# Optimization experiments

Hardware: AMD Instinct MI355X
Metric: run time of the kernel (lower is better)

The kernel has to match this reference:

```python
import jax, jax.numpy as jnp
import numpy as np

D = 768      # hidden_size
H = 12       # num_head
HD = D // H  # head_dim
LN_EPS = 1e-5


def setup_inputs() -> dict:
    key = jax.random.key(0)
    ks = jax.random.split(key, 9)
    N, S = 4, 2048
    s = 0.02
    return {
        "hidden_state": jax.random.normal(ks[0], (N, S, D), dtype=jnp.float32),
        "key_padding_mask": jax.random.randint(ks[1], (N, S), 0, 2, dtype=jnp.int64),
        "Wq": jax.random.normal(ks[2], (D, D), dtype=jnp.float32) * s,
        "Wk": jax.random.normal(ks[3], (D, D), dtype=jnp.float32) * s,
        "Wv": jax.random.normal(ks[4], (D, D), dtype=jnp.float32) * s,
        "Wo": jax.random.normal(ks[5], (D, D), dtype=jnp.float32) * s,
        "W1": jax.random.normal(ks[6], (4 * D, D), dtype=jnp.float32) * s,
        "W2": jax.random.normal(ks[7], (D, 4 * D), dtype=jnp.float32) * s,
        "ln_g": jnp.ones((D,), dtype=jnp.float32),
        "ln_b": jnp.zeros((D,), dtype=jnp.float32),
    }


def _layernorm(x, g, b):
    mu = jnp.mean(x, axis=-1, keepdims=True)
    var = jnp.mean(jnp.square(x - mu), axis=-1, keepdims=True)
    return (x - mu) * jax.lax.rsqrt(var + LN_EPS) * g + b


def reference(hidden_state, key_padding_mask, Wq, Wk, Wv, Wo, W1, W2, ln_g, ln_b):
    x = hidden_state
    N, S, _ = x.shape
    # Note: original module projects K and V from `query` (self-attention).
    def proj(W):
        return (x @ W.T).reshape(N, S, H, HD).transpose(0, 2, 1, 3)  # [N,H,S,HD]
    Q, K, V = proj(Wq), proj(Wk), proj(Wv)
    scores = jnp.einsum("bhqd,bhkd->bhqk", Q, K)  # [N,H,S,S]
    # int mask: 0 marks padding positions -> masked with -inf
    pad = (key_padding_mask == 0)[:, None, None, :]  # [N,1,1,S]
    scores = jnp.where(pad, -jnp.inf, scores)
    attn = jax.nn.softmax(scores / np.sqrt(HD), axis=-1)
    ctx = jnp.einsum("bhqk,bhkd->bhqd", attn, V)
    ctx = ctx.transpose(0, 2, 1, 3).reshape(N, S, D)
    mha = ctx @ Wo.T
    # residual + LayerNorm (same LN params used twice, as in the original)
    n1 = _layernorm(x + mha, ln_g, ln_b)
    # FFN with exact GELU (torch nn.GELU default)
    f = jax.nn.gelu(n1 @ W1.T, approximate=False) @ W2.T
    return _layernorm(n1 + f, ln_g, ln_b)
```

## Files before the change

kernel.cpp:

```cpp
#include <hip/hip_runtime.h>
#include <math.h>

typedef unsigned short u16;
typedef unsigned int u32;
typedef __bf16 bf16x8 __attribute__((ext_vector_type(8)));
typedef float f32x4 __attribute__((ext_vector_type(4)));

#define NB 4
#define SS 2048
#define DD 768
#define HH 12
#define HD 64
#define ROWS (NB*SS)

__device__ __forceinline__ u16 f2bf(float f) {
    union { float f; unsigned u; } v; v.f = f;
    unsigned r = v.u + 0x7fffu + ((v.u >> 16) & 1u);
    return (u16)(r >> 16);
}
__device__ __forceinline__ u32 fas(float f) { union { float f; u32 u; } v; v.f = f; return v.u; }

__device__ __forceinline__ void gl_lds16(const void* g, void* l) {
    __builtin_amdgcn_global_load_lds((__attribute__((address_space(1))) void*)(g),
                                     (__attribute__((address_space(3))) void*)(l),
                                     16, 0, 0);
}

__global__ __launch_bounds__(256) void prep_kernel(
        const float* __restrict__ X, const float* __restrict__ Wq,
        const float* __restrict__ Wk, const float* __restrict__ Wv,
        const float* __restrict__ Wo, const float* __restrict__ W1,
        const float* __restrict__ W2, const int* __restrict__ mask,
        u16* __restrict__ Xb, u16* __restrict__ Wqkvb, u16* __restrict__ Wob,
        u16* __restrict__ W1b, u16* __restrict__ W2b, float* __restrict__ mb) {
    const int blk = blockIdx.x, tid = threadIdx.x;
    const float* src; u16* dst; int idx;
    if (blk < 6144)       { src = X;  dst = Xb;               idx = blk * 1024 + tid * 4; }
    else if (blk < 6720)  { src = Wq; dst = Wqkvb;            idx = (blk - 6144) * 1024 + tid * 4; }
    else if (blk < 7296)  { src = Wk; dst = Wqkvb + DD * DD;  idx = (blk - 6720) * 1024 + tid * 4; }
    else if (blk < 7872)  { src = Wv; dst = Wqkvb + 2*DD*DD;  idx = (blk - 7296) * 1024 + tid * 4; }
    else if (blk < 8448)  { src = Wo; dst = Wob;              idx = (blk - 7872) * 1024 + tid * 4; }
    else if (blk < 10752) { src = W1; dst = W1b;              idx = (blk - 8448) * 1024 + tid * 4; }
    else if (blk < 13056) { src = W2; dst = W2b;              idx = (blk - 10752) * 1024 + tid * 4; }
    else {
        int i = (blk - 13056) * 1024 + tid * 4;
        float4 o;
        o.x = mask[i]     == 0 ? -1e30f : 0.0f;
        o.y = mask[i + 1] == 0 ? -1e30f : 0.0f;
        o.z = mask[i + 2] == 0 ? -1e30f : 0.0f;
        o.w = mask[i + 3] == 0 ? -1e30f : 0.0f;
        *(float4*)&mb[i] = o;
        return;
    }
    float4 v = *(const float4*)&src[idx];
    ushort4 o;
    o.x = f2bf(v.x); o.y = f2bf(v.y); o.z = f2bf(v.z); o.w = f2bf(v.w);
    *(ushort4*)&dst[idx] = o;
}

template <int EPI, int BN>
__global__ __launch_bounds__(256) void gemm_bt(const u16* __restrict__ A,
                                               const u16* __restrict__ B,
                                               int M, int N, int K,
                                               void* __restrict__ out,
                                               const void* __restrict__ aux,
                                               u16* __restrict__ Qb,
                                               u16* __restrict__ Kb,
                                               u16* __restrict__ Vb) {
    __shared__ __align__(16) u16 lA[128 * 64];
    __shared__ __align__(16) u16 lB[BN * 64];
    constexpr int MI = (BN == 128) ? 4 : 2;
    const int tid = threadIdx.x;
    const int lane = tid & 63, wave = tid >> 6;
    const int quad = lane >> 4, lc = lane & 15;
    const int xcd = blockIdx.x & 7, loc = blockIdx.x >> 3;
    const int mb = xcd * 8 + (loc & 7), nb = loc >> 3;
    const int m0 = mb * 128, n0 = nb * BN;
    const int wrow = (BN == 128) ? (wave >> 1) * 64 : wave * 32;
    const int wcol = (BN == 128) ? (wave & 1) * 64 : 0;
    const int swz = lc & 7;

    f32x4 acc[MI][4] = {};

    for (int kb = 0; kb < K; kb += 64) {
        __syncthreads();
#pragma unroll
        for (int p0 = 0; p0 < 1024; p0 += 256) {
            int p = p0 + tid, row = p >> 3, cl = (p & 7) ^ (row & 7);
            gl_lds16(A + (size_t)(m0 + row) * K + kb + cl * 8, &lA[(size_t)(p0 + wave * 64) * 8]);
        }
#pragma unroll
        for (int p0 = 0; p0 < BN * 8; p0 += 256) {
            int p = p0 + tid, row = p >> 3, cl = (p & 7) ^ (row & 7);
            gl_lds16(B + (size_t)(n0 + row) * K + kb + cl * 8, &lB[(size_t)(p0 + wave * 64) * 8]);
        }
        __syncthreads();
#pragma unroll
        for (int k2 = 0; k2 < 2; ++k2) {
            bf16x8 af[MI], bfr[4];
#pragma unroll
            for (int t = 0; t < MI; ++t)
                af[t] = *(const bf16x8*)&lA[(wrow + t * 16 + lc) * 64 + ((quad + k2 * 4) ^ swz) * 8];
#pragma unroll
            for (int t = 0; t < 4; ++t)
                bfr[t] = *(const bf16x8*)&lB[(wcol + t * 16 + lc) * 64 + ((quad + k2 * 4) ^ swz) * 8];
#pragma unroll
            for (int mi = 0; mi < MI; ++mi)
#pragma unroll
                for (int ni = 0; ni < 4; ++ni)
                    acc[mi][ni] = __builtin_amdgcn_mfma_f32_16x16x32_bf16(af[mi], bfr[ni],
                                                                         acc[mi][ni], 0, 0, 0);
        }
    }

#pragma unroll
    for (int mi = 0; mi < MI; ++mi) {
#pragma unroll
        for (int r = 0; r < 4; ++r) {
            int m = m0 + wrow + mi * 16 + quad * 4 + r;
#pragma unroll
            for (int ni = 0; ni < 4; ++ni) {
                int n = n0 + wcol + ni * 16 + lc;
                float v = acc[mi][ni][r];
                if constexpr (EPI == 0) {
                    int b = m >> 11, s = m & 2047;
                    int which = n / DD, rem = n - which * DD;
                    int h = rem >> 6, d = rem & 63;
                    u16* dst = which == 0 ? Qb : (which == 1 ? Kb : Vb);
                    dst[((((size_t)b * HH + h) * SS + s) << 6) + d] = f2bf(v);
                } else if constexpr (EPI == 1) {
                    float u = v * fmaf(v * v, 0.035677408f, 0.7978845608f);
                    float e = __builtin_amdgcn_exp2f(u * 2.885390082f);
                    float g = v - v * __builtin_amdgcn_rcpf(e + 1.0f);
                    ((u16*)out)[(size_t)m * N + n] = f2bf(g);
                } else if constexpr (EPI == 2) {
                    ((float*)out)[(size_t)m * N + n] =
                        v + ((const float*)aux)[(size_t)m * N + n];
                } else {
                    ((float*)out)[(size_t)m * N + n] =
                        v + (float)(((const __bf16*)aux)[(size_t)m * N + n]);
                }
            }
        }
    }
}

__global__ __launch_bounds__(256) void transpose_v(const u16* __restrict__ V,
                                                   u16* __restrict__ Vt) {
    __shared__ u16 t[32][33];
    int bh = blockIdx.z;
    int s0 = blockIdx.x * 32, d0 = blockIdx.y * 32;
    const u16* vb = V + (size_t)bh * SS * HD;
    u16* vtb = Vt + (size_t)bh * HD * SS;
    int tx = threadIdx.x & 31, ty = threadIdx.x >> 5;
#pragma unroll
    for (int i = 0; i < 32; i += 8) t[ty + i][tx] = vb[(size_t)(s0 + ty + i) * HD + d0 + tx];
    __syncthreads();
#pragma unroll
    for (int i = 0; i < 32; i += 8) vtb[(size_t)(d0 + ty + i) * SS + s0 + tx] = t[tx][ty + i];
}

__global__ __launch_bounds__(256) void attn_kernel(const u16* __restrict__ Q,
                                                   const u16* __restrict__ K,
                                                   const u16* __restrict__ Vt,
                                                   const float* __restrict__ maskbias,
                                                   u16* __restrict__ Ctx) {
    __shared__ __align__(16) u16 lK[64 * 64];
    __shared__ __align__(16) u16 lV[64 * 64];
    __shared__ __align__(16) u16 lP[4][32 * 72];
    const int tid = threadIdx.x, lane = tid & 63, wave = tid >> 6;
    const int quad = lane >> 4, lc = lane & 15;
    const int bh = blockIdx.x % (NB * HH);
    const int b = bh / HH, h = bh - b * HH;
    const int q0 = (blockIdx.x / (NB * HH)) * 128;
    const u16* Qg = Q + ((size_t)bh * SS + q0 + wave * 32) * HD;
    const u16* Kg = K + (size_t)bh * SS * HD;
    const u16* Vg = Vt + (size_t)bh * HD * SS;
    const float* mbg = maskbias + b * SS;
    const int sw = lc & 7;

    const int srow = tid >> 3, scl = (tid & 7) ^ (srow & 7);
    const int srow2 = (256 + tid) >> 3, scl2 = (tid & 7) ^ (srow2 & 7);

    bf16x8 qf[2][2];
#pragma unroll
    for (int mi = 0; mi < 2; ++mi)
#pragma unroll
        for (int k2 = 0; k2 < 2; ++k2)
            qf[mi][k2] = *(const bf16x8*)(Qg + (size_t)(mi * 16 + lc) * HD + k2 * 32 + quad * 8);

    bf16x8 onesf;
#pragma unroll
    for (int i = 0; i < 8; ++i) onesf[i] = (__bf16)1.0f;

    f32x4 oacc[2][4] = {};
    f32x4 lsum[2] = {};

    for (int j0 = 0; j0 < SS; j0 += 64) {
        __syncthreads();
        gl_lds16(Kg + (size_t)(j0 + srow) * HD + scl * 8,   &lK[(size_t)(wave * 64) * 8]);
        gl_lds16(Vg + (size_t)srow * SS + j0 + scl * 8,     &lV[(size_t)(wave * 64) * 8]);
        gl_lds16(Kg + (size_t)(j0 + srow2) * HD + scl2 * 8, &lK[(size_t)(256 + wave * 64) * 8]);
        gl_lds16(Vg + (size_t)srow2 * SS + j0 + scl2 * 8,   &lV[(size_t)(256 + wave * 64) * 8]);
        __syncthreads();

        f32x4 sacc[4][2] = {};
#pragma unroll
        for (int k2 = 0; k2 < 2; ++k2)
#pragma unroll
            for (int ni = 0; ni < 4; ++ni) {
                bf16x8 kf = *(const bf16x8*)&lK[(ni * 16 + lc) * 64 + ((quad + k2 * 4) ^ sw) * 8];
                sacc[ni][0] = __builtin_amdgcn_mfma_f32_16x16x32_bf16(kf, qf[0][k2], sacc[ni][0], 0, 0, 0);
                sacc[ni][1] = __builtin_amdgcn_mfma_f32_16x16x32_bf16(kf, qf[1][k2], sacc[ni][1], 0, 0, 0);
            }

#pragma unroll
        for (int ni = 0; ni < 4; ++ni) {
            f32x4 mbv = *(const f32x4*)(mbg + j0 + ni * 16 + quad * 4);
#pragma unroll
            for (int mi = 0; mi < 2; ++mi) {
#pragma unroll
                for (int r = 0; r < 4; ++r)
                    sacc[ni][mi][r] = __builtin_amdgcn_exp2f(fmaf(sacc[ni][mi][r], 0.180336880f, mbv[r]));
                u32 w0 = __builtin_amdgcn_perm(fas(sacc[ni][mi][1]), fas(sacc[ni][mi][0]), 0x07060302);
                u32 w1 = __builtin_amdgcn_perm(fas(sacc[ni][mi][3]), fas(sacc[ni][mi][2]), 0x07060302);
                *(uint2*)&lP[wave][(mi * 16 + lc) * 72 + ni * 16 + quad * 4] = make_uint2(w0, w1);
            }
        }

#pragma unroll
        for (int k2 = 0; k2 < 2; ++k2) {
            bf16x8 pf0 = *(const bf16x8*)&lP[wave][(size_t)lc * 72 + k2 * 32 + quad * 8];
            bf16x8 pf1 = *(const bf16x8*)&lP[wave][(size_t)(16 + lc) * 72 + k2 * 32 + quad * 8];
            lsum[0] = __builtin_amdgcn_mfma_f32_16x16x32_bf16(pf0, onesf, lsum[0], 0, 0, 0);
            lsum[1] = __builtin_amdgcn_mfma_f32_16x16x32_bf16(pf1, onesf, lsum[1], 0, 0, 0);
#pragma unroll
            for (int ni = 0; ni < 4; ++ni) {
                bf16x8 vf = *(const bf16x8*)&lV[(ni * 16 + lc) * 64 + ((quad + k2 * 4) ^ sw) * 8];
                oacc[0][ni] = __builtin_amdgcn_mfma_f32_16x16x32_bf16(pf0, vf, oacc[0][ni], 0, 0, 0);
                oacc[1][ni] = __builtin_amdgcn_mfma_f32_16x16x32_bf16(pf1, vf, oacc[1][ni], 0, 0, 0);
            }
        }
    }

#pragma unroll
    for (int mi = 0; mi < 2; ++mi)
#pragma unroll
        for (int r = 0; r < 4; ++r) {
            float inv = 1.0f / lsum[mi][r];
            int s = q0 + wave * 32 + mi * 16 + quad * 4 + r;
            size_t base = ((size_t)(b * SS + s)) * DD + h * HD;
#pragma unroll
            for (int ni = 0; ni < 4; ++ni)
                Ctx[base + ni * 16 + lc] = f2bf(oacc[mi][ni][r] * inv);
        }
}

__global__ __launch_bounds__(256) void ln_kernel(const float* __restrict__ in,
                                                 const float* __restrict__ g,
                                                 const float* __restrict__ bb,
                                                 u16* __restrict__ out_bf,
                                                 float* __restrict__ out_f) {
    const int row = blockIdx.x, tid = threadIdx.x;
    const float* x = in + (size_t)row * DD;
    float v0 = x[tid], v1 = x[tid + 256], v2 = x[tid + 512];
    float s = v0 + v1 + v2;
    float q = v0 * v0 + v1 * v1 + v2 * v2;
#pragma unroll
    for (int o = 1; o < 64; o <<= 1) {
        s += __shfl_xor(s, o);
        q += __shfl_xor(q, o);
    }
    __shared__ float rs[4], rq[4];
    int wave = tid >> 6;
    if ((tid & 63) == 0) { rs[wave] = s; rq[wave] = q; }
    __syncthreads();
    s = rs[0] + rs[1] + rs[2] + rs[3];
    q = rq[0] + rq[1] + rq[2] + rq[3];
    float mu = s * (1.0f / DD);
    float var = q * (1.0f / DD) - mu * mu;
    float rstd = rsqrtf(var + 1e-5f);
#pragma unroll
    for (int j = 0; j < 3; ++j) {
        int col = tid + j * 256;
        float v = (j == 0 ? v0 : (j == 1 ? v1 : v2));
        float y = (v - mu) * rstd * g[col] + bb[col];
        if (out_bf) out_bf[(size_t)row * DD + col] = f2bf(y);
        if (out_f) out_f[(size_t)row * DD + col] = y;
    }
}

extern "C" void kernel_launch(void* const* d_in, const int* in_sizes, int n_in,
                              void* d_out, int out_size, void* d_ws, size_t ws_size,
                              hipStream_t stream) {
    const float* X    = (const float*)d_in[0];
    const int*   mask = (const int*)d_in[1];
    const float* Wq   = (const float*)d_in[2];
    const float* Wk   = (const float*)d_in[3];
    const float* Wv   = (const float*)d_in[4];
    const float* Wo   = (const float*)d_in[5];
    const float* W1   = (const float*)d_in[6];
    const float* W2   = (const float*)d_in[7];
    const float* ln_g = (const float*)d_in[8];
    const float* ln_b = (const float*)d_in[9];
    float* out = (float*)d_out;

    char* ws = (char*)d_ws;
    size_t off = 0;
    auto alloc = [&](size_t bytes) {
        void* p = ws + off;
        off += (bytes + 255) & ~(size_t)255;
        return p;
    };
    u16*   Xbf   = (u16*)alloc((size_t)ROWS * DD * 2);
    u16*   Wqkvb = (u16*)alloc((size_t)3 * DD * DD * 2);
    u16*   Wob   = (u16*)alloc((size_t)DD * DD * 2);
    u16*   W1b   = (u16*)alloc((size_t)4 * DD * DD * 2);
    u16*   W2b   = (u16*)alloc((size_t)4 * DD * DD * 2);
    float* mbias = (float*)alloc((size_t)NB * SS * 4);
    u16*   Qb    = (u16*)alloc((size_t)ROWS * DD * 2);
    u16*   Kb    = (u16*)alloc((size_t)ROWS * DD * 2);
    u16*   Vb    = (u16*)alloc((size_t)ROWS * DD * 2);
    u16*   Vtb   = (u16*)alloc((size_t)ROWS * DD * 2);
    float* resid = (float*)alloc((size_t)ROWS * DD * 4);
    u16*   n1b   = (u16*)alloc((size_t)ROWS * DD * 2);
    u16*   Gb    = Qb;
    u16*   Ctxb  = Xbf;
    float* h2    = resid;

    prep_kernel<<<dim3(13064), dim3(256), 0, stream>>>(
        X, Wq, Wk, Wv, Wo, W1, W2, mask,
        Xbf, Wqkvb, Wob, W1b, W2b, mbias);

    gemm_bt<0, 128><<<dim3((3 * DD / 128) * (ROWS / 128)), dim3(256), 0, stream>>>(
        Xbf, Wqkvb, ROWS, 3 * DD, DD, nullptr, nullptr, Qb, Kb, Vb);

    transpose_v<<<dim3(SS / 32, HD / 32, NB * HH), dim3(256), 0, stream>>>(Vb, Vtb);

    attn_kernel<<<dim3((SS / 128) * (NB * HH)), dim3(256), 0, stream>>>(
        Qb, Kb, Vtb, mbias, Ctxb);

    gemm_bt<2, 64><<<dim3((DD / 64) * (ROWS / 128)), dim3(256), 0, stream>>>(
        Ctxb, Wob, ROWS, DD, DD, resid, X, nullptr, nullptr, nullptr);

    ln_kernel<<<dim3(ROWS), dim3(256), 0, stream>>>(resid, ln_g, ln_b, n1b, nullptr);

    gemm_bt<1, 128><<<dim3((4 * DD / 128) * (ROWS / 128)), dim3(256), 0, stream>>>(
        n1b, W1b, ROWS, 4 * DD, DD, Gb, nullptr, nullptr, nullptr, nullptr);

    gemm_bt<3, 64><<<dim3((DD / 64) * (ROWS / 128)), dim3(256), 0, stream>>>(
        Gb, W2b, ROWS, DD, 4 * DD, h2, n1b, nullptr, nullptr, nullptr);

    ln_kernel<<<dim3(ROWS), dim3(256), 0, stream>>>(h2, ln_g, ln_b, nullptr, out);
}
```

Measured before the change: 364.7 us.

## Use 8 waves per attention block and pass P through permlane swaps instead of LDS

```diff
diff --git a/kernel.cpp b/kernel.cpp
--- a/kernel.cpp
+++ b/kernel.cpp
@@ -5,6 +5,7 @@
 typedef unsigned int u32;
 typedef __bf16 bf16x8 __attribute__((ext_vector_type(8)));
 typedef float f32x4 __attribute__((ext_vector_type(4)));
+typedef u32 u32x4 __attribute__((ext_vector_type(4)));
 
 #define NB 4
 #define SS 2048
@@ -160,100 +161,96 @@
     for (int i = 0; i < 32; i += 8) vtb[(size_t)(d0 + ty + i) * SS + s0 + tx] = t[tx][ty + i];
 }
 
-__global__ __launch_bounds__(256) void attn_kernel(const u16* __restrict__ Q,
-                                                   const u16* __restrict__ K,
-                                                   const u16* __restrict__ Vt,
-                                                   const float* __restrict__ maskbias,
-                                                   u16* __restrict__ Ctx) {
+__global__ __launch_bounds__(512, 6) void attn_kernel(const u16* __restrict__ Q,
+                                                      const u16* __restrict__ K,
+                                                      const u16* __restrict__ Vt,
+                                                      const float* __restrict__ maskbias,
+                                                      u16* __restrict__ Ctx) {
     __shared__ __align__(16) u16 lK[64 * 64];
     __shared__ __align__(16) u16 lV[64 * 64];
-    __shared__ __align__(16) u16 lP[4][32 * 72];
     const int tid = threadIdx.x, lane = tid & 63, wave = tid >> 6;
     const int quad = lane >> 4, lc = lane & 15;
     const int bh = blockIdx.x % (NB * HH);
     const int b = bh / HH, h = bh - b * HH;
     const int q0 = (blockIdx.x / (NB * HH)) * 128;
-    const u16* Qg = Q + ((size_t)bh * SS + q0 + wave * 32) * HD;
+    const u16* Qg = Q + ((size_t)bh * SS + q0 + wave * 16) * HD;
     const u16* Kg = K + (size_t)bh * SS * HD;
     const u16* Vg = Vt + (size_t)bh * HD * SS;
     const float* mbg = maskbias + b * SS;
     const int sw = lc & 7;
 
     const int srow = tid >> 3, scl = (tid & 7) ^ (srow & 7);
-    const int srow2 = (256 + tid) >> 3, scl2 = (tid & 7) ^ (srow2 & 7);
-
-    bf16x8 qf[2][2];
-#pragma unroll
-    for (int mi = 0; mi < 2; ++mi)
-#pragma unroll
-        for (int k2 = 0; k2 < 2; ++k2)
-            qf[mi][k2] = *(const bf16x8*)(Qg + (size_t)(mi * 16 + lc) * HD + k2 * 32 + quad * 8);
+
+    bf16x8 qf[2];
+#pragma unroll
+    for (int k2 = 0; k2 < 2; ++k2)
+        qf[k2] = *(const bf16x8*)(Qg + (size_t)lc * HD + k2 * 32 + quad * 8);
 
     bf16x8 onesf;
 #pragma unroll
     for (int i = 0; i < 8; ++i) onesf[i] = (__bf16)1.0f;
 
-    f32x4 oacc[2][4] = {};
-    f32x4 lsum[2] = {};
+    f32x4 oacc[4] = {};
+    f32x4 lsum = {};
 
     for (int j0 = 0; j0 < SS; j0 += 64) {
         __syncthreads();
-        gl_lds16(Kg + (size_t)(j0 + srow) * HD + scl * 8,   &lK[(size_t)(wave * 64) * 8]);
-        gl_lds16(Vg + (size_t)srow * SS + j0 + scl * 8,     &lV[(size_t)(wave * 64) * 8]);
-        gl_lds16(Kg + (size_t)(j0 + srow2) * HD + scl2 * 8, &lK[(size_t)(256 + wave * 64) * 8]);
-        gl_lds16(Vg + (size_t)srow2 * SS + j0 + scl2 * 8,   &lV[(size_t)(256 + wave * 64) * 8]);
+        gl_lds16(Kg + (size_t)(j0 + srow) * HD + scl * 8, &lK[(size_t)(wave * 64) * 8]);
+        gl_lds16(Vg + (size_t)srow * SS + j0 + scl * 8,   &lV[(size_t)(wave * 64) * 8]);
         __syncthreads();
 
-        f32x4 sacc[4][2] = {};
+        f32x4 sacc[4] = {};
+        __builtin_amdgcn_s_setprio(1);
 #pragma unroll
         for (int k2 = 0; k2 < 2; ++k2)
 #pragma unroll
             for (int ni = 0; ni < 4; ++ni) {
                 bf16x8 kf = *(const bf16x8*)&lK[(ni * 16 + lc) * 64 + ((quad + k2 * 4) ^ sw) * 8];
-                sacc[ni][0] = __builtin_amdgcn_mfma_f32_16x16x32_bf16(kf, qf[0][k2], sacc[ni][0], 0, 0, 0);
-                sacc[ni][1] = __builtin_amdgcn_mfma_f32_16x16x32_bf16(kf, qf[1][k2], sacc[ni][1], 0, 0, 0);
+                sacc[ni] = __builtin_amdgcn_mfma_f32_16x16x32_bf16(kf, qf[k2], sacc[ni], 0, 0, 0);
             }
-
+        __builtin_amdgcn_s_setprio(0);
+
+        u32 pa[4], pb[4];
 #pragma unroll
         for (int ni = 0; ni < 4; ++ni) {
             f32x4 mbv = *(const f32x4*)(mbg + j0 + ni * 16 + quad * 4);
 #pragma unroll
-            for (int mi = 0; mi < 2; ++mi) {
-#pragma unroll
-                for (int r = 0; r < 4; ++r)
-                    sacc[ni][mi][r] = __builtin_amdgcn_exp2f(fmaf(sacc[ni][mi][r], 0.180336880f, mbv[r]));
-                u32 w0 = __builtin_amdgcn_perm(fas(sacc[ni][mi][1]), fas(sacc[ni][mi][0]), 0x07060302);
-                u32 w1 = __builtin_amdgcn_perm(fas(sacc[ni][mi][3]), fas(sacc[ni][mi][2]), 0x07060302);
-                *(uint2*)&lP[wave][(mi * 16 + lc) * 72 + ni * 16 + quad * 4] = make_uint2(w0, w1);
-            }
+            for (int r = 0; r < 4; ++r)
+                sacc[ni][r] = __builtin_amdgcn_exp2f(fmaf(sacc[ni][r], 0.180336880f, mbv[r]));
+            pa[ni] = __builtin_amdgcn_perm(fas(sacc[ni][1]), fas(sacc[ni][0]), 0x07060302);
+            pb[ni] = __builtin_amdgcn_perm(fas(sacc[ni][3]), fas(sacc[ni][2]), 0x07060302);
         }
 
 #pragma unroll
         for (int k2 = 0; k2 < 2; ++k2) {
-            bf16x8 pf0 = *(const bf16x8*)&lP[wave][(size_t)lc * 72 + k2 * 32 + quad * 8];
-            bf16x8 pf1 = *(const bf16x8*)&lP[wave][(size_t)(16 + lc) * 72 + k2 * 32 + quad * 8];
-            lsum[0] = __builtin_amdgcn_mfma_f32_16x16x32_bf16(pf0, onesf, lsum[0], 0, 0, 0);
-            lsum[1] = __builtin_amdgcn_mfma_f32_16x16x32_bf16(pf1, onesf, lsum[1], 0, 0, 0);
+            u32 xa = pa[2 * k2], ya = pa[2 * k2 + 1];
+            u32 xb = pb[2 * k2], yb = pb[2 * k2 + 1];
+            asm("v_permlane32_swap_b32 %0, %1" : "+v"(xa), "+v"(ya));
+            asm("v_permlane16_swap_b32 %0, %1" : "+v"(xa), "+v"(ya));
+            asm("v_permlane32_swap_b32 %0, %1" : "+v"(xb), "+v"(yb));
+            asm("v_permlane16_swap_b32 %0, %1" : "+v"(xb), "+v"(yb));
+            u32x4 pw = { xa, xb, ya, yb };
+            bf16x8 pf = __builtin_bit_cast(bf16x8, pw);
+            __builtin_amdgcn_s_setprio(1);
+            lsum = __builtin_amdgcn_mfma_f32_16x16x32_bf16(pf, onesf, lsum, 0, 0, 0);
 #pragma unroll
             for (int ni = 0; ni < 4; ++ni) {
                 bf16x8 vf = *(const bf16x8*)&lV[(ni * 16 + lc) * 64 + ((quad + k2 * 4) ^ sw) * 8];
-                oacc[0][ni] = __builtin_amdgcn_mfma_f32_16x16x32_bf16(pf0, vf, oacc[0][ni], 0, 0, 0);
-                oacc[1][ni] = __builtin_amdgcn_mfma_f32_16x16x32_bf16(pf1, vf, oacc[1][ni], 0, 0, 0);
+                oacc[ni] = __builtin_amdgcn_mfma_f32_16x16x32_bf16(pf, vf, oacc[ni], 0, 0, 0);
             }
-        }
-    }
-
-#pragma unroll
-    for (int mi = 0; mi < 2; ++mi)
-#pragma unroll
-        for (int r = 0; r < 4; ++r) {
-            float inv = 1.0f / lsum[mi][r];
-            int s = q0 + wave * 32 + mi * 16 + quad * 4 + r;
-            size_t base = ((size_t)(b * SS + s)) * DD + h * HD;
-#pragma unroll
-            for (int ni = 0; ni < 4; ++ni)
-                Ctx[base + ni * 16 + lc] = f2bf(oacc[mi][ni][r] * inv);
-        }
+            __builtin_amdgcn_s_setprio(0);
+        }
+    }
+
+#pragma unroll
+    for (int r = 0; r < 4; ++r) {
+        float inv = 1.0f / lsum[r];
+        int s = q0 + wave * 16 + quad * 4 + r;
+        size_t base = ((size_t)(b * SS + s)) * DD + h * HD;
+#pragma unroll
+        for (int ni = 0; ni < 4; ++ni)
+            Ctx[base + ni * 16 + lc] = f2bf(oacc[ni][r] * inv);
+    }
 }
 
 __global__ __launch_bounds__(256) void ln_kernel(const float* __restrict__ in,
@@ -337,7 +334,7 @@
 
     transpose_v<<<dim3(SS / 32, HD / 32, NB * HH), dim3(256), 0, stream>>>(Vb, Vtb);
 
-    attn_kernel<<<dim3((SS / 128) * (NB * HH)), dim3(256), 0, stream>>>(
+    attn_kernel<<<dim3((SS / 128) * (NB * HH)), dim3(512), 0, stream>>>(
         Qb, Kb, Vtb, mbias, Ctxb);
 
     gemm_bt<2, 64><<<dim3((DD / 64) * (ROWS / 128)), dim3(256), 0, stream>>>(
```

Result: no change. 362.5 us (-0.6%).

## Double-buffer K/V tiles and keep P in registers via permlane swaps

Applied to the files above, without the earlier changes.

```diff
diff --git a/kernel.cpp b/kernel.cpp
--- a/kernel.cpp
+++ b/kernel.cpp
@@ -5,6 +5,7 @@
 typedef unsigned int u32;
 typedef __bf16 bf16x8 __attribute__((ext_vector_type(8)));
 typedef float f32x4 __attribute__((ext_vector_type(4)));
+typedef u32 u32x4 __attribute__((ext_vector_type(4)));
 
 #define NB 4
 #define SS 2048
@@ -160,14 +161,13 @@
     for (int i = 0; i < 32; i += 8) vtb[(size_t)(d0 + ty + i) * SS + s0 + tx] = t[tx][ty + i];
 }
 
-__global__ __launch_bounds__(256) void attn_kernel(const u16* __restrict__ Q,
-                                                   const u16* __restrict__ K,
-                                                   const u16* __restrict__ Vt,
-                                                   const float* __restrict__ maskbias,
-                                                   u16* __restrict__ Ctx) {
-    __shared__ __align__(16) u16 lK[64 * 64];
-    __shared__ __align__(16) u16 lV[64 * 64];
-    __shared__ __align__(16) u16 lP[4][32 * 72];
+__global__ __launch_bounds__(256, 3) void attn_kernel(const u16* __restrict__ Q,
+                                                      const u16* __restrict__ K,
+                                                      const u16* __restrict__ Vt,
+                                                      const float* __restrict__ maskbias,
+                                                      u16* __restrict__ Ctx) {
+    __shared__ __align__(16) u16 lK[2][4224];
+    __shared__ __align__(16) u16 lV[2][4096];
     const int tid = threadIdx.x, lane = tid & 63, wave = tid >> 6;
     const int quad = lane >> 4, lc = lane & 15;
     const int bh = blockIdx.x % (NB * HH);
@@ -182,6 +182,14 @@
     const int srow = tid >> 3, scl = (tid & 7) ^ (srow & 7);
     const int srow2 = (256 + tid) >> 3, scl2 = (tid & 7) ^ (srow2 & 7);
 
+    auto stage = [&](int bi, int j0) {
+        gl_lds16(Kg + (size_t)(j0 + srow) * HD + scl * 8,   &lK[bi][(size_t)(wave * 64) * 8]);
+        gl_lds16(Kg + (size_t)(j0 + srow2) * HD + scl2 * 8, &lK[bi][(size_t)(256 + wave * 64) * 8]);
+        gl_lds16(Vg + (size_t)srow * SS + j0 + scl * 8,     &lV[bi][(size_t)(wave * 64) * 8]);
+        gl_lds16(Vg + (size_t)srow2 * SS + j0 + scl2 * 8,   &lV[bi][(size_t)(256 + wave * 64) * 8]);
+        if (lane < 16) gl_lds16(mbg + j0 + lane * 4, &lK[bi][4096]);
+    };
+
     bf16x8 qf[2][2];
 #pragma unroll
     for (int mi = 0; mi < 2; ++mi)
@@ -196,51 +204,86 @@
     f32x4 oacc[2][4] = {};
     f32x4 lsum[2] = {};
 
-    for (int j0 = 0; j0 < SS; j0 += 64) {
-        __syncthreads();
-        gl_lds16(Kg + (size_t)(j0 + srow) * HD + scl * 8,   &lK[(size_t)(wave * 64) * 8]);
-        gl_lds16(Vg + (size_t)srow * SS + j0 + scl * 8,     &lV[(size_t)(wave * 64) * 8]);
-        gl_lds16(Kg + (size_t)(j0 + srow2) * HD + scl2 * 8, &lK[(size_t)(256 + wave * 64) * 8]);
-        gl_lds16(Vg + (size_t)srow2 * SS + j0 + scl2 * 8,   &lV[(size_t)(256 + wave * 64) * 8]);
-        __syncthreads();
-
-        f32x4 sacc[4][2] = {};
-#pragma unroll
-        for (int k2 = 0; k2 < 2; ++k2)
+    stage(0, 0);
+    for (int t = 0; t < SS / 64; ++t) {
+        const int cur = t & 1;
+        if (t < SS / 64 - 1) {
+            stage(cur ^ 1, (t + 1) * 64);
+            __builtin_amdgcn_sched_barrier(0);
+            asm volatile("s_waitcnt vmcnt(5)" ::: "memory");
+        } else {
+            __builtin_amdgcn_sched_barrier(0);
+            asm volatile("s_waitcnt vmcnt(0)" ::: "memory");
+        }
+        __builtin_amdgcn_sched_barrier(0);
+        __builtin_amdgcn_s_barrier();
+        __builtin_amdgcn_sched_barrier(0);
+
+        const u16* bK = &lK[cur][0];
+        const u16* bV = &lV[cur][0];
+        const float* bM = (const float*)&lK[cur][4096];
+
+        f32x4 sacc[2][4] = {};
+        __builtin_amdgcn_s_setprio(1);
+#pragma unroll
+        for (int k2 = 0; k2 < 2; ++k2) {
+            bf16x8 kf[4];
+#pragma unroll
+            for (int ni = 0; ni < 4; ++ni)
+                kf[ni] = *(const bf16x8*)&bK[(ni * 16 + lc) * 64 + ((quad + k2 * 4) ^ sw) * 8];
 #pragma unroll
             for (int ni = 0; ni < 4; ++ni) {
-                bf16x8 kf = *(const bf16x8*)&lK[(ni * 16 + lc) * 64 + ((quad + k2 * 4) ^ sw) * 8];
-                sacc[ni][0] = __builtin_amdgcn_mfma_f32_16x16x32_bf16(kf, qf[0][k2], sacc[ni][0], 0, 0, 0);
-                sacc[ni][1] = __builtin_amdgcn_mfma_f32_16x16x32_bf16(kf, qf[1][k2], sacc[ni][1], 0, 0, 0);
-            }
-
+                sacc[0][ni] = __builtin_amdgcn_mfma_f32_16x16x32_bf16(kf[ni], qf[0][k2], sacc[0][ni], 0, 0, 0);
+                sacc[1][ni] = __builtin_amdgcn_mfma_f32_16x16x32_bf16(kf[ni], qf[1][k2], sacc[1][ni], 0, 0, 0);
+            }
+        }
+        __builtin_amdgcn_s_setprio(0);
+
+        u32 pa[2][4], pb[2][4];
 #pragma unroll
         for (int ni = 0; ni < 4; ++ni) {
-            f32x4 mbv = *(const f32x4*)(mbg + j0 + ni * 16 + quad * 4);
+            f32x4 mbv = *(const f32x4*)&bM[ni * 16 + quad * 4];
 #pragma unroll
             for (int mi = 0; mi < 2; ++mi) {
 #pragma unroll
                 for (int r = 0; r < 4; ++r)
-                    sacc[ni][mi][r] = __builtin_amdgcn_exp2f(fmaf(sacc[ni][mi][r], 0.180336880f, mbv[r]));
-                u32 w0 = __builtin_amdgcn_perm(fas(sacc[ni][mi][1]), fas(sacc[ni][mi][0]), 0x07060302);
-                u32 w1 = __builtin_amdgcn_perm(fas(sacc[ni][mi][3]), fas(sacc[ni][mi][2]), 0x07060302);
-                *(uint2*)&lP[wave][(mi * 16 + lc) * 72 + ni * 16 + quad * 4] = make_uint2(w0, w1);
-            }
-        }
-
+                    sacc[mi][ni][r] = __builtin_amdgcn_exp2f(fmaf(sacc[mi][ni][r], 0.180336880f, mbv[r]));
+                pa[mi][ni] = __builtin_amdgcn_perm(fas(sacc[mi][ni][1]), fas(sacc[mi][ni][0]), 0x07060302);
+                pb[mi][ni] = __builtin_amdgcn_perm(fas(sacc[mi][ni][3]), fas(sacc[mi][ni][2]), 0x07060302);
+            }
+        }
+
+        bf16x8 pf[2][2];
+#pragma unroll
+        for (int mi = 0; mi < 2; ++mi)
+#pragma unroll
+            for (int k2 = 0; k2 < 2; ++k2) {
+                u32 xa = pa[mi][2 * k2], ya = pa[mi][2 * k2 + 1];
+                u32 xb = pb[mi][2 * k2], yb = pb[mi][2 * k2 + 1];
+                asm("v_permlane32_swap_b32 %0, %1" : "+v"(xa), "+v"(ya));
+                asm("v_permlane16_swap_b32 %0, %1" : "+v"(xa), "+v"(ya));
+                asm("v_permlane32_swap_b32 %0, %1" : "+v"(xb), "+v"(yb));
+                asm("v_permlane16_swap_b32 %0, %1" : "+v"(xb), "+v"(yb));
+                u32x4 pw = { xa, xb, ya, yb };
+                pf[mi][k2] = __builtin_bit_cast(bf16x8, pw);
+            }
+
+        __builtin_amdgcn_s_setprio(1);
 #pragma unroll
         for (int k2 = 0; k2 < 2; ++k2) {
-            bf16x8 pf0 = *(const bf16x8*)&lP[wave][(size_t)lc * 72 + k2 * 32 + quad * 8];
-            bf16x8 pf1 = *(const bf16x8*)&lP[wave][(size_t)(16 + lc) * 72 + k2 * 32 + quad * 8];
-            lsum[0] = __builtin_amdgcn_mfma_f32_16x16x32_bf16(pf0, onesf, lsum[0], 0, 0, 0);
-            lsum[1] = __builtin_amdgcn_mfma_f32_16x16x32_bf16(pf1, onesf, lsum[1], 0, 0, 0);
+            lsum[0] = __builtin_amdgcn_mfma_f32_16x16x32_bf16(pf[0][k2], onesf, lsum[0], 0, 0, 0);
+            lsum[1] = __builtin_amdgcn_mfma_f32_16x16x32_bf16(pf[1][k2], onesf, lsum[1], 0, 0, 0);
 #pragma unroll
             for (int ni = 0; ni < 4; ++ni) {
-                bf16x8 vf = *(const bf16x8*)&lV[(ni * 16 + lc) * 64 + ((quad + k2 * 4) ^ sw) * 8];
-                oacc[0][ni] = __builtin_amdgcn_mfma_f32_16x16x32_bf16(pf0, vf, oacc[0][ni], 0, 0, 0);
-                oacc[1][ni] = __builtin_amdgcn_mfma_f32_16x16x32_bf16(pf1, vf, oacc[1][ni], 0, 0, 0);
-            }
-        }
+                bf16x8 vf = *(const bf16x8*)&bV[(ni * 16 + lc) * 64 + ((quad + k2 * 4) ^ sw) * 8];
+                oacc[0][ni] = __builtin_amdgcn_mfma_f32_16x16x32_bf16(pf[0][k2], vf, oacc[0][ni], 0, 0, 0);
+                oacc[1][ni] = __builtin_amdgcn_mfma_f32_16x16x32_bf16(pf[1][k2], vf, oacc[1][ni], 0, 0, 0);
+            }
+        }
+        __builtin_amdgcn_s_setprio(0);
+
+        __builtin_amdgcn_sched_barrier(0);
+        __builtin_amdgcn_s_barrier();
     }
 
 #pragma unroll
```

New measurement: 354.4 us. 2.8% less time.
